# Performance work log

Hardware: AMD Instinct MI355X
Metric: run time of the kernel (lower is better)

Reference implementation:

```python
import jax, jax.numpy as jnp
import numpy as np

N_QUBITS = 6
BLOCKS = 3
LATENT = 3
DIM = 1 << N_QUBITS  # 64, state-vector size
BATCH = 131072
INP_DIM = 6  # must equal N_QUBITS (repo applies linear_pre to the n_qubits-dim recon)

# Wire 0 is the most-significant qubit (PennyLane convention).
_idx = np.arange(DIM)
BITS = ((_idx[:, None] >> (N_QUBITS - 1 - np.arange(N_QUBITS))) & 1)  # (64, 6)
# Chain of CZ(k, k+1): all diagonal, fold into one sign vector per block.
CZ_SIGN = jnp.asarray(np.prod(1 - 2 * (BITS[:, :-1] * BITS[:, 1:]), axis=1).astype(np.float32))  # (64,)
Z_SIGNS = jnp.asarray((1 - 2 * BITS).astype(np.float32))  # (64, 6): <Z_k> signs per basis state


def _apply_1q(state, U, wire):
    # state: (B, 64) complex64; U: (2,2) complex64 acting on `wire`
    B = state.shape[0]
    s = state.reshape(B, 1 << wire, 2, 1 << (N_QUBITS - 1 - wire))
    s = jnp.einsum('ij,bxjy->bxiy', U, s)
    return s.reshape(B, DIM)


def _circuit(amps, weights, n_out):
    # AmplitudeEmbedding with normalize=True (x was already unit-normed in torch; idempotent)
    norm = jnp.linalg.norm(amps, axis=1, keepdims=True)
    state = (amps / norm).astype(jnp.complex64)  # (B, 64)
    for j in range(BLOCKS):
        for k in range(N_QUBITS):
            tx = weights[j, k, 0]
            tz = weights[j, k, 1]
            c = jnp.cos(0.5 * tx).astype(jnp.complex64)
            s = jnp.sin(0.5 * tx).astype(jnp.complex64)
            em = jnp.exp(-0.5j * tz).astype(jnp.complex64)
            ep = jnp.exp(0.5j * tz).astype(jnp.complex64)
            # Fused U = RZ(tz) @ RX(tx)
            U = jnp.stack([jnp.stack([em * c, -1j * em * s]),
                           jnp.stack([-1j * ep * s, ep * c])])
            state = _apply_1q(state, U, k)
        state = state * CZ_SIGN  # all CZ gates of the block, fused
    probs = state.real ** 2 + state.imag ** 2  # (B, 64)
    return probs @ Z_SIGNS[:, :n_out]  # expval(PauliZ(k)) for k < n_out


def setup_inputs() -> dict:
    key = jax.random.key(0)
    k1, k2, k3, k4, k5 = jax.random.split(key, 5)
    x = jax.random.normal(k1, (BATCH, INP_DIM), dtype=jnp.float32)
    bound = 1.0 / np.sqrt(INP_DIM)
    W_pre = jax.random.uniform(k2, (DIM, INP_DIM), minval=-bound, maxval=bound, dtype=jnp.float32)
    b_pre = jax.random.uniform(k3, (DIM,), minval=-bound, maxval=bound, dtype=jnp.float32)
    enc_w = jax.random.normal(k4, (BLOCKS, N_QUBITS, 3), dtype=jnp.float32) * 0.01
    dec_w = jax.random.normal(k5, (BLOCKS, N_QUBITS, 3), dtype=jnp.float32) * 0.01
    return {'x': x, 'W_pre': W_pre, 'b_pre': b_pre, 'enc_w': enc_w, 'dec_w': dec_w}


def reference(x, W_pre, b_pre, enc_w, dec_w):
    h = jnp.tanh(x @ W_pre.T + b_pre)                     # (B, 64)
    latent = _circuit(h, enc_w, LATENT)                    # (B, 3)
    padded = jnp.zeros((x.shape[0], DIM), jnp.float32).at[:, :LATENT].set(latent)
    recon = _circuit(padded, dec_w, N_QUBITS)              # (B, 6)
    reconstructed = jnp.tanh(recon @ W_pre.T + b_pre)      # (B, 64)
    return reconstructed, latent
```

## Files before the change

kernel.cpp:

```cpp
#include <hip/hip_runtime.h>

#define BATCH 131072

typedef float v2f __attribute__((ext_vector_type(2)));


__device__ __forceinline__ float fast_tanh(float v) {
    float e = __expf(2.0f * v);
    return 1.0f - 2.0f / (e + 1.0f);
}

template <int CTRL>
__device__ __forceinline__ float dppf(float v) {
    return __int_as_float(__builtin_amdgcn_update_dpp(
        0, __float_as_int(v), CTRL, 0xF, 0xF, true));
}
#define DPP_XOR1 0xB1
#define DPP_XOR2 0x4E

__device__ __forceinline__ v2f swap2(v2f v) { return __builtin_shufflevector(v, v, 1, 0); }

__global__ __launch_bounds__(256) void prep_kernel(const float* __restrict__ enc_w,
                                                   const float* __restrict__ dec_w,
                                                   float* __restrict__ ws) {
    __shared__ float gt[18][8];
    __shared__ float Sr[64][8];
    __shared__ float Si[64][8];
    const int t = threadIdx.x;

    if (t < 18) {
        float tx = dec_w[t * 3 + 0];
        float tz = dec_w[t * 3 + 1];
        float c = cosf(0.5f * tx), s = sinf(0.5f * tx);
        float ch = cosf(0.5f * tz), sh = sinf(0.5f * tz);
        gt[t][0] = c * ch;  gt[t][1] = -c * sh;
        gt[t][2] = -s * sh; gt[t][3] = -s * ch;
        gt[t][4] = s * sh;  gt[t][5] = -s * ch;
        gt[t][6] = c * ch;  gt[t][7] = c * sh;
    }

    const int cl = t & 7;
    const int pr = t >> 3;
    float* fSr = &Sr[0][0];
    float* fSi = &Si[0][0];
    for (int f = t; f < 512; f += 256) {
        int r = f >> 3, c = f & 7;
        fSr[f] = (r == c && c < 3) ? 1.0f : 0.0f;
        fSi[f] = 0.0f;
    }

    for (int bb = 0; bb < 3; ++bb) {
        for (int w = 0; w < 6; ++w) {
            __syncthreads();
            int g = bb * 6 + w;
            int p = 5 - w;
            float u00r = gt[g][0], u00i = gt[g][1], u01r = gt[g][2], u01i = gt[g][3];
            float u10r = gt[g][4], u10i = gt[g][5], u11r = gt[g][6], u11i = gt[g][7];
            int r0 = ((pr >> p) << (p + 1)) | (pr & ((1 << p) - 1));
            int r1 = r0 | (1 << p);
            float ar = Sr[r0][cl], ai = Si[r0][cl];
            float br = Sr[r1][cl], bi = Si[r1][cl];
            Sr[r0][cl] = u00r * ar - u00i * ai + u01r * br - u01i * bi;
            Si[r0][cl] = u00r * ai + u00i * ar + u01r * bi + u01i * br;
            Sr[r1][cl] = u10r * ar - u10i * ai + u11r * br - u11i * bi;
            Si[r1][cl] = u10r * ai + u10i * ar + u11r * bi + u11i * br;
        }
        __syncthreads();
        for (int f = t; f < 512; f += 256) {
            int r = f >> 3;
            if (__popc(r & (r >> 1)) & 1) {
                fSr[f] = -fSr[f];
                fSi[f] = -fSi[f];
            }
        }
    }
    __syncthreads();

    if (t < 36) {
        int k = t / 6, i = t % 6;
        int d = (i < 3) ? i : ((i == 5) ? 1 : 0);
        int e = (i < 3) ? i : ((i == 3) ? 1 : 2);
        float acc = 0.0f;
        for (int r = 0; r < 64; ++r) {
            float term = Sr[r][d] * Sr[r][e] + Si[r][d] * Si[r][e];
            acc += ((r >> (5 - k)) & 1) ? -term : term;
        }
        if (i >= 3) acc *= 2.0f;
        ws[t] = acc;
    }

    if (t < 18) {
        float tx = enc_w[t * 3 + 0];
        float c = cosf(0.5f * tx), s = sinf(0.5f * tx);
        if (t >= 12) {
            ws[64 + 2 * t] = c * c - s * s;
            ws[65 + 2 * t] = 4.0f * c * s;
        } else {
            ws[64 + 2 * t] = c;
            ws[65 + 2 * t] = s;
        }
    }

    if (t >= 64 && t < 256) {
        int idx = t - 64;
        int bb = idx >> 6, r = idx & 63;
        float phi = 0.0f;
        for (int k = 0; k < 6; ++k) {
            float tz = enc_w[(bb * 6 + k) * 3 + 1];
            phi += ((r >> (5 - k)) & 1) ? 0.5f * tz : -0.5f * tz;
        }
        float sgn = (__popc(r & (r >> 1)) & 1) ? -1.0f : 1.0f;
        ws[128 + bb * 128 + 2 * r] = sgn * cosf(phi);
        ws[129 + bb * 128 + 2 * r] = sgn * sinf(phi);
    }
}

template <int MASK>
__device__ __forceinline__ void rx_pairs(v2f* zr, v2f* zi, float c, float s) {
#pragma unroll
    for (int j = 0; j < 8; ++j) {
        if (j & MASK) continue;
        int j1 = j | MASK;
        v2f ar = zr[j], ai = zi[j], br = zr[j1], bi = zi[j1];
        zr[j]  = c * ar + s * bi;
        zi[j]  = c * ai - s * br;
        zr[j1] = c * br + s * ai;
        zi[j1] = c * bi - s * ar;
    }
}

template <int CTRL>
__device__ __forceinline__ void rx_exch2(v2f* zr, v2f* zi, float c, float s) {
#pragma unroll
    for (int j = 0; j < 8; ++j) {
        v2f pr, pi;
        pr.x = dppf<CTRL>(zr[j].x);
        pr.y = dppf<CTRL>(zr[j].y);
        pi.x = dppf<CTRL>(zi[j].x);
        pi.y = dppf<CTRL>(zi[j].y);
        v2f mr = zr[j], mi = zi[j];
        zr[j] = c * mr + s * pi;
        zi[j] = c * mi - s * pr;
    }
}

__global__ __launch_bounds__(256) void qae_main(const float* __restrict__ x,
                                                const float* __restrict__ Wp,
                                                const float* __restrict__ bp,
                                                const float* __restrict__ ws,
                                                float* __restrict__ out) {
    __shared__ float sW[540];
    __shared__ float sD[256];
    __shared__ float sLat[192];

    const int t = threadIdx.x;
    const int bl = t >> 2;
    const int sub = t & 3;

    for (int f = t; f < 512; f += 256) {
        int g = f >> 4, e = f & 15;
        int j = g >> 2, su = g & 3;
        float val;
        if (e < 12)      { int row = 8 * j + su + 4 * (e & 1); val = Wp[row * 6 + (e >> 1)]; }
        else if (e < 14) { int row = 8 * j + su + 4 * (e - 12); val = bp[row]; }
        else val = 0.0f;
        sW[g * 16 + j * 4 + e] = val;
    }
    if (t < 128) {
        int bb = t >> 6, r = t & 63;
        int su = r & 3, m = r >> 2, j = m >> 1, hm = m & 1;
        int base = ((bb * 8 + j) * 4 + su) * 4;
        sD[base + hm]     = ws[128 + bb * 128 + 2 * r];
        sD[base + 2 + hm] = ws[128 + bb * 128 + 2 * r + 1];
    }
    __syncthreads();

    const size_t b = (size_t)blockIdx.x * 64 + bl;
    const float* xp = x + b * 6;
    float2 x01 = *(const float2*)(xp);
    float2 x23 = *(const float2*)(xp + 2);
    float2 x45 = *(const float2*)(xp + 4);
    float xv[6] = {x01.x, x01.y, x23.x, x23.y, x45.x, x45.y};

    v2f zr[8], zi[8];
    v2f S2 = {0.0f, 0.0f};
#pragma unroll
    for (int j = 0; j < 8; ++j) {
        const float* wb = &sW[(j * 4 + sub) * 16 + j * 4];
        float4 c0 = *(const float4*)wb;
        float4 c1 = *(const float4*)(wb + 4);
        float4 c2 = *(const float4*)(wb + 8);
        float4 c3 = *(const float4*)(wb + 12);
        v2f a = {c3.x, c3.y};
        a += xv[0] * (v2f){c0.x, c0.y};
        a += xv[1] * (v2f){c0.z, c0.w};
        a += xv[2] * (v2f){c1.x, c1.y};
        a += xv[3] * (v2f){c1.z, c1.w};
        a += xv[4] * (v2f){c2.x, c2.y};
        a += xv[5] * (v2f){c2.z, c2.w};
        v2f th = {fast_tanh(a.x), fast_tanh(a.y)};
        zr[j] = th;
        zi[j] = (v2f){0.0f, 0.0f};
        S2 += th * th;
    }
    float S = S2.x + S2.y;
    S += dppf<DPP_XOR1>(S);
    S += dppf<DPP_XOR2>(S);
    float invS = __builtin_amdgcn_rcpf(S);

#pragma unroll 1
    for (int bb = 0; bb < 2; ++bb) {
        const float* rx = ws + 64 + 12 * bb;
        rx_pairs<4>(zr, zi, rx[0], rx[1]);
        rx_pairs<2>(zr, zi, rx[2], rx[3]);
        rx_pairs<1>(zr, zi, rx[4], rx[5]);
        {
            float c = rx[6], s = rx[7];
#pragma unroll
            for (int j = 0; j < 8; ++j) {
                v2f orr = zr[j], oi = zi[j];
                zr[j] = c * orr + s * swap2(oi);
                zi[j] = c * oi - s * swap2(orr);
            }
        }
        rx_exch2<DPP_XOR2>(zr, zi, rx[8], rx[9]);
        rx_exch2<DPP_XOR1>(zr, zi, rx[10], rx[11]);
#pragma unroll
        for (int j = 0; j < 8; ++j) {
            float4 d = *(const float4*)&sD[((bb * 8 + j) * 4 + sub) * 4];
            v2f dr = {d.x, d.y}, di = {d.z, d.w};
            v2f orr = zr[j], oi = zi[j];
            zr[j] = dr * orr - di * oi;
            zi[j] = dr * oi + di * orr;
        }
    }

    v2f L0 = {0, 0}, L1 = {0, 0}, L2 = {0, 0};
#pragma unroll
    for (int j = 0; j < 8; ++j) {
        v2f p = zr[j] * zr[j] + zi[j] * zi[j];
        L0 += (j & 4) ? -p : p;
        L1 += (j & 2) ? -p : p;
        L2 += (j & 1) ? -p : p;
    }
    v2f Y0 = {0, 0}, Y1 = {0, 0}, Y2 = {0, 0};
#pragma unroll
    for (int j = 0; j < 4; ++j)
        Y0 += zr[j] * zi[j | 4] - zi[j] * zr[j | 4];
#pragma unroll
    for (int j0 = 0; j0 < 8; j0 += 4)
#pragma unroll
        for (int j = j0; j < j0 + 2; ++j)
            Y1 += zr[j] * zi[j | 2] - zi[j] * zr[j | 2];
#pragma unroll
    for (int j = 0; j < 8; j += 2)
        Y2 += zr[j] * zi[j | 1] - zi[j] * zr[j | 1];

    float l0 = L0.x + L0.y, l1 = L1.x + L1.y, l2 = L2.x + L2.y;
    float y0 = Y0.x + Y0.y, y1 = Y1.x + Y1.y, y2 = Y2.x + Y2.y;
    l0 += dppf<DPP_XOR1>(l0); l0 += dppf<DPP_XOR2>(l0);
    l1 += dppf<DPP_XOR1>(l1); l1 += dppf<DPP_XOR2>(l1);
    l2 += dppf<DPP_XOR1>(l2); l2 += dppf<DPP_XOR2>(l2);
    y0 += dppf<DPP_XOR1>(y0); y0 += dppf<DPP_XOR2>(y0);
    y1 += dppf<DPP_XOR1>(y1); y1 += dppf<DPP_XOR2>(y1);
    y2 += dppf<DPP_XOR1>(y2); y2 += dppf<DPP_XOR2>(y2);

    const float* p2 = ws + 88;
    l0 = (p2[0] * l0 + p2[1] * y0) * invS;
    l1 = (p2[2] * l1 + p2[3] * y1) * invS;
    l2 = (p2[4] * l2 + p2[5] * y2) * invS;

    float q0 = l0 * l0, q1 = l1 * l1, q2 = l2 * l2;
    float q3 = l0 * l1, q4 = l0 * l2, q5 = l1 * l2;
    float r2 = q0 + q1 + q2;
    float invr2 = __builtin_amdgcn_rcpf(r2);
    float rec[6];
#pragma unroll
    for (int k = 0; k < 6; ++k) {
        const float* A = ws + k * 6;
        float acc = A[0] * q0 + A[1] * q1 + A[2] * q2
                  + A[3] * q3 + A[4] * q4 + A[5] * q5;
        rec[k] = acc * invr2;
    }

    if (sub == 0) {
        sLat[bl * 3 + 0] = l0;
        sLat[bl * 3 + 1] = l1;
        sLat[bl * 3 + 2] = l2;
    }
    __syncthreads();
    if (t < 192) out[(size_t)BATCH * 64 + (size_t)blockIdx.x * 192 + t] = sLat[t];

    const size_t ob = b * 64;
#pragma unroll
    for (int jj = 0; jj < 2; ++jj) {
        int jrow = 2 * sub + jj;
        float vlo[4], vhi[4];
#pragma unroll
        for (int su2 = 0; su2 < 4; ++su2) {
            int g = jrow * 4 + su2;
            const float* wb = &sW[g * 16 + jrow * 4];
            float4 c0 = *(const float4*)wb;
            float4 c1 = *(const float4*)(wb + 4);
            float4 c2 = *(const float4*)(wb + 8);
            float2 b2 = *(const float2*)(wb + 12);
            v2f a = {b2.x, b2.y};
            a += rec[0] * (v2f){c0.x, c0.y};
            a += rec[1] * (v2f){c0.z, c0.w};
            a += rec[2] * (v2f){c1.x, c1.y};
            a += rec[3] * (v2f){c1.z, c1.w};
            a += rec[4] * (v2f){c2.x, c2.y};
            a += rec[5] * (v2f){c2.z, c2.w};
            vlo[su2] = fast_tanh(a.x);
            vhi[su2] = fast_tanh(a.y);
        }
        float4 o0 = {vlo[0], vlo[1], vlo[2], vlo[3]};
        float4 o1 = {vhi[0], vhi[1], vhi[2], vhi[3]};
        *(float4*)&out[ob + 8 * jrow]     = o0;
        *(float4*)&out[ob + 8 * jrow + 4] = o1;
    }
}

extern "C" void kernel_launch(void* const* d_in, const int* in_sizes, int n_in,
                              void* d_out, int out_size, void* d_ws, size_t ws_size,
                              hipStream_t stream) {
    const float* x   = (const float*)d_in[0];
    const float* Wp  = (const float*)d_in[1];
    const float* bpv = (const float*)d_in[2];
    const float* enc = (const float*)d_in[3];
    const float* dec = (const float*)d_in[4];
    float* out = (float*)d_out;
    float* ws  = (float*)d_ws;

    prep_kernel<<<1, 256, 0, stream>>>(enc, dec, ws);
    qae_main<<<(BATCH * 4) / 256, 256, 0, stream>>>(x, Wp, bpv, ws, out);
}
```

Baseline: 101.8 us.

## Fold decoder quadratic form into W_pre and stream outputs directly

The prep kernel now pre-multiplies W_pre by the decoder quadratic-form coefficients, so each output row becomes a 6-term dot product with normalized quadratic monomials plus bias. The main kernel stages this fused table in LDS and writes 16 contiguous outputs per lane. The latent output is written directly to global memory, which drops the LDS staging and the block barrier. Smaller changes ride along: the first RX layer is specialized for the zero imaginary part, the projection coefficients are applied before the DPP reductions so there are fewer shuffles, the x loads are hoisted above the LDS fill, and launch bounds request 4 blocks per CU. The latent stores become strided 3-float writes, which may coalesce less well.

```diff
diff --git a/kernel.cpp b/kernel.cpp
--- a/kernel.cpp
+++ b/kernel.cpp
@@ -22,10 +22,13 @@
 
 __global__ __launch_bounds__(256) void prep_kernel(const float* __restrict__ enc_w,
                                                    const float* __restrict__ dec_w,
+                                                   const float* __restrict__ Wp,
+                                                   const float* __restrict__ bp,
                                                    float* __restrict__ ws) {
     __shared__ float gt[18][8];
     __shared__ float Sr[64][8];
     __shared__ float Si[64][8];
+    __shared__ float sA[36];
     const int t = threadIdx.x;
 
     if (t < 18) {
@@ -86,7 +89,7 @@
             acc += ((r >> (5 - k)) & 1) ? -term : term;
         }
         if (i >= 3) acc *= 2.0f;
-        ws[t] = acc;
+        sA[t] = acc;
     }
 
     if (t < 18) {
@@ -113,6 +116,20 @@
         ws[128 + bb * 128 + 2 * r] = sgn * cosf(phi);
         ws[129 + bb * 128 + 2 * r] = sgn * sinf(phi);
     }
+    __syncthreads();
+
+    if (t < 64) {
+        float w0 = Wp[t * 6 + 0], w1 = Wp[t * 6 + 1], w2 = Wp[t * 6 + 2];
+        float w3 = Wp[t * 6 + 3], w4 = Wp[t * 6 + 4], w5 = Wp[t * 6 + 5];
+#pragma unroll
+        for (int i = 0; i < 6; ++i) {
+            float acc = w0 * sA[0 * 6 + i] + w1 * sA[1 * 6 + i] + w2 * sA[2 * 6 + i]
+                      + w3 * sA[3 * 6 + i] + w4 * sA[4 * 6 + i] + w5 * sA[5 * 6 + i];
+            ws[512 + t * 8 + i] = acc;
+        }
+        ws[512 + t * 8 + 6] = bp[t];
+        ws[512 + t * 8 + 7] = 0.0f;
+    }
 }
 
 template <int MASK>
@@ -144,18 +161,49 @@
     }
 }
 
-__global__ __launch_bounds__(256) void qae_main(const float* __restrict__ x,
-                                                const float* __restrict__ Wp,
-                                                const float* __restrict__ bp,
-                                                const float* __restrict__ ws,
-                                                float* __restrict__ out) {
+__device__ __forceinline__ void enc_tail(v2f* zr, v2f* zi, const float* rx,
+                                         const float* sDblk, int sub) {
+    rx_pairs<2>(zr, zi, rx[2], rx[3]);
+    rx_pairs<1>(zr, zi, rx[4], rx[5]);
+    {
+        float c = rx[6], s = rx[7];
+#pragma unroll
+        for (int j = 0; j < 8; ++j) {
+            v2f orr = zr[j], oi = zi[j];
+            zr[j] = c * orr + s * swap2(oi);
+            zi[j] = c * oi - s * swap2(orr);
+        }
+    }
+    rx_exch2<DPP_XOR2>(zr, zi, rx[8], rx[9]);
+    rx_exch2<DPP_XOR1>(zr, zi, rx[10], rx[11]);
+#pragma unroll
+    for (int j = 0; j < 8; ++j) {
+        float4 d = *(const float4*)&sDblk[(j * 4 + sub) * 4];
+        v2f dr = {d.x, d.y}, di = {d.z, d.w};
+        v2f orr = zr[j], oi = zi[j];
+        zr[j] = dr * orr - di * oi;
+        zi[j] = dr * oi + di * orr;
+    }
+}
+
+__global__ __launch_bounds__(256, 4) void qae_main(const float* __restrict__ x,
+                                                   const float* __restrict__ Wp,
+                                                   const float* __restrict__ bp,
+                                                   const float* __restrict__ ws,
+                                                   float* __restrict__ out) {
     __shared__ float sW[540];
+    __shared__ float sB[544];
     __shared__ float sD[256];
-    __shared__ float sLat[192];
 
     const int t = threadIdx.x;
     const int bl = t >> 2;
     const int sub = t & 3;
+
+    const size_t b = (size_t)blockIdx.x * 64 + bl;
+    const float* xp = x + b * 6;
+    float2 x01 = *(const float2*)(xp);
+    float2 x23 = *(const float2*)(xp + 2);
+    float2 x45 = *(const float2*)(xp + 4);
 
     for (int f = t; f < 512; f += 256) {
         int g = f >> 4, e = f & 15;
@@ -166,6 +214,9 @@
         else val = 0.0f;
         sW[g * 16 + j * 4 + e] = val;
     }
+    for (int f = t; f < 512; f += 256) {
+        sB[f + ((f >> 7) << 2)] = ws[512 + f];
+    }
     if (t < 128) {
         int bb = t >> 6, r = t & 63;
         int su = r & 3, m = r >> 2, j = m >> 1, hm = m & 1;
@@ -175,11 +226,6 @@
     }
     __syncthreads();
 
-    const size_t b = (size_t)blockIdx.x * 64 + bl;
-    const float* xp = x + b * 6;
-    float2 x01 = *(const float2*)(xp);
-    float2 x23 = *(const float2*)(xp + 2);
-    float2 x45 = *(const float2*)(xp + 4);
     float xv[6] = {x01.x, x01.y, x23.x, x23.y, x45.x, x45.y};
 
     v2f zr[8], zi[8];
@@ -200,7 +246,6 @@
         a += xv[5] * (v2f){c2.z, c2.w};
         v2f th = {fast_tanh(a.x), fast_tanh(a.y)};
         zr[j] = th;
-        zi[j] = (v2f){0.0f, 0.0f};
         S2 += th * th;
     }
     float S = S2.x + S2.y;
@@ -208,31 +253,23 @@
     S += dppf<DPP_XOR2>(S);
     float invS = __builtin_amdgcn_rcpf(S);
 
-#pragma unroll 1
-    for (int bb = 0; bb < 2; ++bb) {
-        const float* rx = ws + 64 + 12 * bb;
+    {
+        const float* rx = ws + 64;
+        float c = rx[0], s = rx[1];
+#pragma unroll
+        for (int j = 0; j < 4; ++j) {
+            v2f a = zr[j], b2 = zr[j + 4];
+            zr[j]     = c * a;
+            zi[j]     = -s * b2;
+            zr[j + 4] = c * b2;
+            zi[j + 4] = -s * a;
+        }
+        enc_tail(zr, zi, rx, sD, sub);
+    }
+    {
+        const float* rx = ws + 76;
         rx_pairs<4>(zr, zi, rx[0], rx[1]);
-        rx_pairs<2>(zr, zi, rx[2], rx[3]);
-        rx_pairs<1>(zr, zi, rx[4], rx[5]);
-        {
-            float c = rx[6], s = rx[7];
-#pragma unroll
-            for (int j = 0; j < 8; ++j) {
-                v2f orr = zr[j], oi = zi[j];
-                zr[j] = c * orr + s * swap2(oi);
-                zi[j] = c * oi - s * swap2(orr);
-            }
-        }
-        rx_exch2<DPP_XOR2>(zr, zi, rx[8], rx[9]);
-        rx_exch2<DPP_XOR1>(zr, zi, rx[10], rx[11]);
-#pragma unroll
-        for (int j = 0; j < 8; ++j) {
-            float4 d = *(const float4*)&sD[((bb * 8 + j) * 4 + sub) * 4];
-            v2f dr = {d.x, d.y}, di = {d.z, d.w};
-            v2f orr = zr[j], oi = zi[j];
-            zr[j] = dr * orr - di * oi;
-            zi[j] = dr * oi + di * orr;
-        }
+        enc_tail(zr, zi, rx, sD + 128, sub);
     }
 
     v2f L0 = {0, 0}, L1 = {0, 0}, L2 = {0, 0};
@@ -256,68 +293,44 @@
     for (int j = 0; j < 8; j += 2)
         Y2 += zr[j] * zi[j | 1] - zi[j] * zr[j | 1];
 
-    float l0 = L0.x + L0.y, l1 = L1.x + L1.y, l2 = L2.x + L2.y;
-    float y0 = Y0.x + Y0.y, y1 = Y1.x + Y1.y, y2 = Y2.x + Y2.y;
-    l0 += dppf<DPP_XOR1>(l0); l0 += dppf<DPP_XOR2>(l0);
-    l1 += dppf<DPP_XOR1>(l1); l1 += dppf<DPP_XOR2>(l1);
-    l2 += dppf<DPP_XOR1>(l2); l2 += dppf<DPP_XOR2>(l2);
-    y0 += dppf<DPP_XOR1>(y0); y0 += dppf<DPP_XOR2>(y0);
-    y1 += dppf<DPP_XOR1>(y1); y1 += dppf<DPP_XOR2>(y1);
-    y2 += dppf<DPP_XOR1>(y2); y2 += dppf<DPP_XOR2>(y2);
-
     const float* p2 = ws + 88;
-    l0 = (p2[0] * l0 + p2[1] * y0) * invS;
-    l1 = (p2[2] * l1 + p2[3] * y1) * invS;
-    l2 = (p2[4] * l2 + p2[5] * y2) * invS;
+    float t0 = p2[0] * (L0.x + L0.y) + p2[1] * (Y0.x + Y0.y);
+    float t1 = p2[2] * (L1.x + L1.y) + p2[3] * (Y1.x + Y1.y);
+    float t2 = p2[4] * (L2.x + L2.y) + p2[5] * (Y2.x + Y2.y);
+    t0 += dppf<DPP_XOR1>(t0); t0 += dppf<DPP_XOR2>(t0);
+    t1 += dppf<DPP_XOR1>(t1); t1 += dppf<DPP_XOR2>(t1);
+    t2 += dppf<DPP_XOR1>(t2); t2 += dppf<DPP_XOR2>(t2);
+    float l0 = t0 * invS, l1 = t1 * invS, l2 = t2 * invS;
+
+    if (sub == 0) {
+        size_t lo = (size_t)BATCH * 64 + b * 3;
+        out[lo]     = l0;
+        out[lo + 1] = l1;
+        out[lo + 2] = l2;
+    }
 
     float q0 = l0 * l0, q1 = l1 * l1, q2 = l2 * l2;
-    float q3 = l0 * l1, q4 = l0 * l2, q5 = l1 * l2;
-    float r2 = q0 + q1 + q2;
-    float invr2 = __builtin_amdgcn_rcpf(r2);
-    float rec[6];
-#pragma unroll
-    for (int k = 0; k < 6; ++k) {
-        const float* A = ws + k * 6;
-        float acc = A[0] * q0 + A[1] * q1 + A[2] * q2
-                  + A[3] * q3 + A[4] * q4 + A[5] * q5;
-        rec[k] = acc * invr2;
-    }
-
-    if (sub == 0) {
-        sLat[bl * 3 + 0] = l0;
-        sLat[bl * 3 + 1] = l1;
-        sLat[bl * 3 + 2] = l2;
-    }
-    __syncthreads();
-    if (t < 192) out[(size_t)BATCH * 64 + (size_t)blockIdx.x * 192 + t] = sLat[t];
-
-    const size_t ob = b * 64;
-#pragma unroll
-    for (int jj = 0; jj < 2; ++jj) {
-        int jrow = 2 * sub + jj;
-        float vlo[4], vhi[4];
-#pragma unroll
-        for (int su2 = 0; su2 < 4; ++su2) {
-            int g = jrow * 4 + su2;
-            const float* wb = &sW[g * 16 + jrow * 4];
-            float4 c0 = *(const float4*)wb;
-            float4 c1 = *(const float4*)(wb + 4);
-            float4 c2 = *(const float4*)(wb + 8);
-            float2 b2 = *(const float2*)(wb + 12);
-            v2f a = {b2.x, b2.y};
-            a += rec[0] * (v2f){c0.x, c0.y};
-            a += rec[1] * (v2f){c0.z, c0.w};
-            a += rec[2] * (v2f){c1.x, c1.y};
-            a += rec[3] * (v2f){c1.z, c1.w};
-            a += rec[4] * (v2f){c2.x, c2.y};
-            a += rec[5] * (v2f){c2.z, c2.w};
-            vlo[su2] = fast_tanh(a.x);
-            vhi[su2] = fast_tanh(a.y);
-        }
-        float4 o0 = {vlo[0], vlo[1], vlo[2], vlo[3]};
-        float4 o1 = {vhi[0], vhi[1], vhi[2], vhi[3]};
-        *(float4*)&out[ob + 8 * jrow]     = o0;
-        *(float4*)&out[ob + 8 * jrow + 4] = o1;
+    float invr2 = __builtin_amdgcn_rcpf(q0 + q1 + q2);
+    float qh0 = q0 * invr2, qh1 = q1 * invr2, qh2 = q2 * invr2;
+    float qh3 = (l0 * l1) * invr2, qh4 = (l0 * l2) * invr2, qh5 = (l1 * l2) * invr2;
+
+    const float* bB = &sB[132 * sub];
+    const size_t ob = b * 64 + 16 * sub;
+#pragma unroll
+    for (int ch = 0; ch < 4; ++ch) {
+        float v4[4];
+#pragma unroll
+        for (int r = 0; r < 4; ++r) {
+            int qq = ch * 4 + r;
+            float4 u0 = *(const float4*)&bB[8 * qq];
+            float4 u1 = *(const float4*)&bB[8 * qq + 4];
+            float acc = u1.z
+                      + qh0 * u0.x + qh1 * u0.y + qh2 * u0.z + qh3 * u0.w
+                      + qh4 * u1.x + qh5 * u1.y;
+            v4[r] = fast_tanh(acc);
+        }
+        float4 o = {v4[0], v4[1], v4[2], v4[3]};
+        *(float4*)&out[ob + ch * 4] = o;
     }
 }
 
@@ -332,6 +345,6 @@
     float* out = (float*)d_out;
     float* ws  = (float*)d_ws;
 
-    prep_kernel<<<1, 256, 0, stream>>>(enc, dec, ws);
+    prep_kernel<<<1, 256, 0, stream>>>(enc, dec, Wp, bpv, ws);
     qae_main<<<(BATCH * 4) / 256, 256, 0, stream>>>(x, Wp, bpv, ws, out);
 }
```

After: 102.2 us. Within noise of the previous version (+0.4%).
